# Kernel optimization log

Hardware: AMD Instinct MI355X
Metric: run time of the kernel (lower is better)

The kernel has to match this reference:

```python
import jax, jax.numpy as jnp
import numpy as np

EMB = 1024
HEADS = 16
HEAD_DIM = EMB // HEADS


def setup_inputs() -> dict:
    key = jax.random.key(0)
    ks = jax.random.split(key, 6)
    B, T, D = 4, 2048, EMB
    s = 1.0 / np.sqrt(D)
    return {
        "x": jax.random.normal(ks[0], (B, T, D), dtype=jnp.float32),
        "Wq": jax.random.normal(ks[1], (D, D), dtype=jnp.float32) * s,
        "Wk": jax.random.normal(ks[2], (D, D), dtype=jnp.float32) * s,
        "Wv": jax.random.normal(ks[3], (D, D), dtype=jnp.float32) * s,
        "Wo": jax.random.normal(ks[4], (D, D), dtype=jnp.float32) * s,
        "bo": jax.random.normal(ks[5], (D,), dtype=jnp.float32) * 0.01,
    }


def reference(x, Wq, Wk, Wv, Wo, bo):
    B, T, D = x.shape
    H, Hd = HEADS, HEAD_DIM
    # torch Linear: x @ W.T ; here W stored [out,in]
    def heads(W):
        return (x @ W.T).reshape(B, T, H, Hd).transpose(0, 2, 1, 3)  # [B,H,T,Hd]
    Q, K, V = heads(Wq), heads(Wk), heads(Wv)
    scores = jnp.einsum("bhqd,bhkd->bhqk", Q, K) / np.sqrt(Hd)
    causal = jnp.triu(jnp.ones((T, T), dtype=bool), k=1)
    scores = jnp.where(causal, -jnp.inf, scores)
    weights = jax.nn.softmax(scores, axis=-1)  # dropout rate 0 -> identity
    ctx = jnp.einsum("bhqk,bhkd->bhqd", weights, V)
    ctx = ctx.transpose(0, 2, 1, 3).reshape(B, T, D)
    return ctx @ Wo.T + bo
```

## Files before the change

### kernel.cpp

```cpp
#include <hip/hip_runtime.h>

typedef short bf16x8 __attribute__((ext_vector_type(8)));
typedef float f32x4 __attribute__((ext_vector_type(4)));
typedef unsigned short u16;
typedef unsigned int u32;

__device__ __forceinline__ u16 f2b(float x) {
  union { float f; u32 u; } c; c.f = x;
  u32 r = (c.u + 0x7FFFu + ((c.u >> 16) & 1u)) >> 16;
  return (u16)r;
}

__device__ __forceinline__ float fexp2(float x) {
  return __builtin_amdgcn_exp2f(x);
}

__device__ __forceinline__ void glds16(const void* g, void* l) {
  __builtin_amdgcn_global_load_lds(
      (const __attribute__((address_space(1))) u32*)g,
      (__attribute__((address_space(3))) u32*)l, 16, 0, 0);
}

__global__ void cvt_kernel(const float* __restrict__ src, u16* __restrict__ dst,
                           int n4, float scale) {
  int i = blockIdx.x * blockDim.x + threadIdx.x;
  if (i >= n4) return;
  float4 v = reinterpret_cast<const float4*>(src)[i];
  ushort4 o;
  o.x = f2b(v.x * scale); o.y = f2b(v.y * scale);
  o.z = f2b(v.z * scale); o.w = f2b(v.w * scale);
  reinterpret_cast<ushort4*>(dst)[i] = o;
}

template<int MODE>
__global__ __launch_bounds__(256, 2)
void gemm_bt(const u16* __restrict__ A, const u16* __restrict__ Bm,
             u16* __restrict__ Cq, u16* __restrict__ Ck, u16* __restrict__ Cv,
             float* __restrict__ Cf, const float* __restrict__ bias, int K) {
  __shared__ __attribute__((aligned(16))) u16 As[128 * 32];
  __shared__ __attribute__((aligned(16))) u16 Bs[128 * 32];
  const int tid = threadIdx.x;
  const int w = tid >> 6, l = tid & 63;
  const int wr = w >> 1, wc = w & 1;
  const int lr = l & 15, lg = l >> 4;
  const int row0 = blockIdx.x * 128;
  const int col0 = blockIdx.y * 128;
  const int sr = l >> 2;
  const int sc = (l & 3) * 8;

  f32x4 acc[4][4] = {};

  for (int kt = 0; kt < K; kt += 32) {
    __syncthreads();
#pragma unroll
    for (int cc = 0; cc < 2; ++cc) {
      const int c = w * 2 + cc;
      glds16(A + (size_t)(row0 + c * 16 + sr) * K + kt + sc, &As[c * 512]);
      glds16(Bm + (size_t)(col0 + c * 16 + sr) * K + kt + sc, &Bs[c * 512]);
    }
    asm volatile("s_waitcnt vmcnt(0)" ::: "memory");
    __syncthreads();

    bf16x8 af[4], bfr[4];
#pragma unroll
    for (int m = 0; m < 4; ++m)
      af[m] = *reinterpret_cast<const bf16x8*>(&As[(wr * 64 + m * 16 + lr) * 32 + lg * 8]);
#pragma unroll
    for (int n = 0; n < 4; ++n)
      bfr[n] = *reinterpret_cast<const bf16x8*>(&Bs[(wc * 64 + n * 16 + lr) * 32 + lg * 8]);
#pragma unroll
    for (int m = 0; m < 4; ++m)
#pragma unroll
      for (int n = 0; n < 4; ++n)
        acc[m][n] = __builtin_amdgcn_mfma_f32_16x16x32_bf16(af[m], bfr[n], acc[m][n], 0, 0, 0);
  }

  if (MODE == 0) {
    const int seg = col0 >> 10;
    u16* dst = (seg == 0) ? Cq : (seg == 1 ? Ck : Cv);
    const int cseg = col0 & 1023;
#pragma unroll
    for (int m = 0; m < 4; ++m) {
      const size_t r = (size_t)(row0 + wr * 64 + m * 16 + lg * 4);
#pragma unroll
      for (int n = 0; n < 4; ++n) {
        const int cg = cseg + wc * 64 + n * 16 + lr;
#pragma unroll
        for (int j = 0; j < 4; ++j)
          dst[(r + j) * 1024 + cg] = f2b(acc[m][n][j]);
      }
    }
  } else {
#pragma unroll
    for (int m = 0; m < 4; ++m) {
      const size_t r = (size_t)(row0 + wr * 64 + m * 16 + lg * 4);
#pragma unroll
      for (int n = 0; n < 4; ++n) {
        const int cg = col0 + wc * 64 + n * 16 + lr;
        const float bv = bias[cg];
#pragma unroll
        for (int j = 0; j < 4; ++j)
          Cf[(r + j) * 1024 + cg] = acc[m][n][j] + bv;
      }
    }
  }
}

__global__ void transpose_v(const u16* __restrict__ vb, u16* __restrict__ vt) {
  __shared__ __attribute__((aligned(16))) u16 Ls[64][72];
  const int bh = blockIdx.x, tb = blockIdx.y;
  const int bb = bh >> 4, h = bh & 15;
  const int t0 = tb * 64;
  const int tid = threadIdx.x;
#pragma unroll
  for (int it = 0; it < 2; ++it) {
    int idx = it * 256 + tid;
    int r = idx >> 3, c8 = (idx & 7) * 8;
    *reinterpret_cast<bf16x8*>(&Ls[r][c8]) =
        *reinterpret_cast<const bf16x8*>(&vb[(size_t)(bb * 2048 + t0 + r) * 1024 + h * 64 + c8]);
  }
  __syncthreads();
#pragma unroll
  for (int it = 0; it < 2; ++it) {
    int idx = it * 256 + tid;
    int d = idx >> 3, c8 = (idx & 7) * 8;
    bf16x8 v;
#pragma unroll
    for (int i = 0; i < 8; ++i) v[i] = (short)Ls[c8 + i][d];
    *reinterpret_cast<bf16x8*>(&vt[(size_t)(bh * 64 + d) * 2048 + t0 + c8]) = v;
  }
}

__global__ __launch_bounds__(256, 3)
void attn_kernel(const u16* __restrict__ qb, const u16* __restrict__ kb,
                 const u16* __restrict__ vt, u16* __restrict__ ctx) {
  __shared__ __attribute__((aligned(16))) u16 Ks[2][64 * 72];
  __shared__ __attribute__((aligned(16))) u16 Vs[2][64 * 72];
  __shared__ __attribute__((aligned(16))) u16 Ps[4 * 32 * 64];
  const int bid = blockIdx.x;
  const int qt = 15 - (bid >> 6);
  const int bh = bid & 63;
  const int bb = bh >> 4, h = bh & 15;
  const int tid = threadIdx.x, w = tid >> 6, l = tid & 63;
  const int lr = l & 15, lg = l >> 4;
  const int Qw = qt * 128 + w * 32;
  const int kvr = tid >> 3;
  const int kvc = (tid & 7) * 8;

  bf16x8 qf[2][2];
#pragma unroll
  for (int mi = 0; mi < 2; ++mi)
#pragma unroll
    for (int kc = 0; kc < 2; ++kc)
      qf[mi][kc] = *reinterpret_cast<const bf16x8*>(
          &qb[(size_t)(bb * 2048 + Qw + mi * 16 + lr) * 1024 + h * 64 + kc * 32 + lg * 8]);

  f32x4 oacc[2][4] = {};
  float lsum[2][4] = {};

  const int ntiles = 2 * qt + 2;

  bf16x8 kr[2], vr[2];
#pragma unroll
  for (int it = 0; it < 2; ++it) {
    kr[it] = *reinterpret_cast<const bf16x8*>(
        &kb[(size_t)(bb * 2048 + it * 32 + kvr) * 1024 + h * 64 + kvc]);
    vr[it] = *reinterpret_cast<const bf16x8*>(
        &vt[(size_t)(bh * 64 + it * 32 + kvr) * 2048 + kvc]);
  }
#pragma unroll
  for (int it = 0; it < 2; ++it) {
    *reinterpret_cast<bf16x8*>(&Ks[0][(it * 32 + kvr) * 72 + kvc]) = kr[it];
    *reinterpret_cast<bf16x8*>(&Vs[0][(it * 32 + kvr) * 72 + kvc]) = vr[it];
  }
  __syncthreads();
#pragma unroll
  for (int it = 0; it < 2; ++it) {
    kr[it] = *reinterpret_cast<const bf16x8*>(
        &kb[(size_t)(bb * 2048 + 64 + it * 32 + kvr) * 1024 + h * 64 + kvc]);
    vr[it] = *reinterpret_cast<const bf16x8*>(
        &vt[(size_t)(bh * 64 + it * 32 + kvr) * 2048 + 64 + kvc]);
  }

  for (int t = 0; t < ntiles; ++t) {
    const int c0 = t * 64;
    const int cur = t & 1;

    if (c0 < Qw + 32) {
      const bool diag = (c0 + 63 > Qw);

      f32x4 sacc[2][4] = {};
      __builtin_amdgcn_s_setprio(1);
#pragma unroll
      for (int kc = 0; kc < 2; ++kc)
#pragma unroll
        for (int nj = 0; nj < 4; ++nj) {
          bf16x8 kf = *reinterpret_cast<const bf16x8*>(
              &Ks[cur][(nj * 16 + lr) * 72 + kc * 32 + lg * 8]);
#pragma unroll
          for (int mi = 0; mi < 2; ++mi)
            sacc[mi][nj] = __builtin_amdgcn_mfma_f32_16x16x32_bf16(qf[mi][kc], kf, sacc[mi][nj], 0, 0, 0);
        }
      __builtin_amdgcn_s_setprio(0);

#pragma unroll
      for (int mi = 0; mi < 2; ++mi) {
        if (diag) {
#pragma unroll
          for (int nj = 0; nj < 4; ++nj) {
            const int col = c0 + nj * 16 + lr;
#pragma unroll
            for (int j = 0; j < 4; ++j) {
              const int row = Qw + mi * 16 + lg * 4 + j;
              if (col > row) sacc[mi][nj][j] = -1e30f;
            }
          }
        }
#pragma unroll
        for (int nj = 0; nj < 4; ++nj) {
          const int cchunk = nj * 2 + (lr >> 3);
          const int coff = lr & 7;
#pragma unroll
          for (int j = 0; j < 4; ++j) {
            const float p = fexp2(sacc[mi][nj][j]);
            lsum[mi][j] += p;
            const int rowP = mi * 16 + lg * 4 + j;
            Ps[w * 2048 + rowP * 64 + ((cchunk ^ (rowP & 7)) * 8) + coff] = f2b(p);
          }
        }
      }

      __builtin_amdgcn_s_setprio(1);
#pragma unroll
      for (int kc = 0; kc < 2; ++kc) {
        bf16x8 pf[2];
#pragma unroll
        for (int mi = 0; mi < 2; ++mi) {
          const int rowP = mi * 16 + lr;
          const int cj = kc * 4 + lg;
          pf[mi] = *reinterpret_cast<const bf16x8*>(
              &Ps[w * 2048 + rowP * 64 + ((cj ^ (rowP & 7)) * 8)]);
        }
#pragma unroll
        for (int nd = 0; nd < 4; ++nd) {
          bf16x8 vf = *reinterpret_cast<const bf16x8*>(
              &Vs[cur][(nd * 16 + lr) * 72 + kc * 32 + lg * 8]);
#pragma unroll
          for (int mi = 0; mi < 2; ++mi)
            oacc[mi][nd] = __builtin_amdgcn_mfma_f32_16x16x32_bf16(pf[mi], vf, oacc[mi][nd], 0, 0, 0);
        }
      }
      __builtin_amdgcn_s_setprio(0);
    }

    if (t + 1 < ntiles) {
#pragma unroll
      for (int it = 0; it < 2; ++it) {
        *reinterpret_cast<bf16x8*>(&Ks[cur ^ 1][(it * 32 + kvr) * 72 + kvc]) = kr[it];
        *reinterpret_cast<bf16x8*>(&Vs[cur ^ 1][(it * 32 + kvr) * 72 + kvc]) = vr[it];
      }
    }
    __syncthreads();
    if (t + 2 < ntiles) {
      const int c0n = c0 + 128;
#pragma unroll
      for (int it = 0; it < 2; ++it) {
        kr[it] = *reinterpret_cast<const bf16x8*>(
            &kb[(size_t)(bb * 2048 + c0n + it * 32 + kvr) * 1024 + h * 64 + kvc]);
        vr[it] = *reinterpret_cast<const bf16x8*>(
            &vt[(size_t)(bh * 64 + it * 32 + kvr) * 2048 + c0n + kvc]);
      }
    }
  }

#pragma unroll
  for (int mi = 0; mi < 2; ++mi) {
#pragma unroll
    for (int x = 1; x < 16; x <<= 1)
#pragma unroll
      for (int j = 0; j < 4; ++j) lsum[mi][j] += __shfl_xor(lsum[mi][j], x, 64);
#pragma unroll
    for (int j = 0; j < 4; ++j) {
      const float inv = 1.0f / lsum[mi][j];
      const size_t r = (size_t)(bb * 2048 + Qw + mi * 16 + lg * 4 + j);
#pragma unroll
      for (int nd = 0; nd < 4; ++nd)
        ctx[r * 1024 + h * 64 + nd * 16 + lr] = f2b(oacc[mi][nd][j] * inv);
    }
  }
}

extern "C" void kernel_launch(void* const* d_in, const int* in_sizes, int n_in,
                              void* d_out, int out_size, void* d_ws, size_t ws_size,
                              hipStream_t stream) {
  const float* x = (const float*)d_in[0];
  const float* Wq = (const float*)d_in[1];
  const float* Wk = (const float*)d_in[2];
  const float* Wv = (const float*)d_in[3];
  const float* Wo = (const float*)d_in[4];
  const float* bo = (const float*)d_in[5];
  float* out = (float*)d_out;

  char* ws = (char*)d_ws;
  u16* xb = (u16*)(ws);
  u16* qb = (u16*)(ws + (16u << 20));
  u16* kb = (u16*)(ws + (32u << 20));
  u16* vb = (u16*)(ws + (48u << 20));
  u16* vtb = (u16*)(ws + (64u << 20));
  u16* wqkvb = (u16*)(ws + (80u << 20));
  u16* wob = (u16*)(ws + (88u << 20));

  const float qscale = 0.125f * 1.4426950408889634f;
  cvt_kernel<<<8192, 256, 0, stream>>>(x, xb, 8388608 / 4, 1.0f);
  cvt_kernel<<<1024, 256, 0, stream>>>(Wq, wqkvb, 1048576 / 4, qscale);
  cvt_kernel<<<1024, 256, 0, stream>>>(Wk, wqkvb + 1048576, 1048576 / 4, 1.0f);
  cvt_kernel<<<1024, 256, 0, stream>>>(Wv, wqkvb + 2097152, 1048576 / 4, 1.0f);
  cvt_kernel<<<1024, 256, 0, stream>>>(Wo, wob, 1048576 / 4, 1.0f);

  gemm_bt<0><<<dim3(64, 24), 256, 0, stream>>>(xb, wqkvb, qb, kb, vb, nullptr, nullptr, 1024);
  transpose_v<<<dim3(64, 32), 256, 0, stream>>>(vb, vtb);
  attn_kernel<<<1024, 256, 0, stream>>>(qb, kb, vtb, xb);
  gemm_bt<1><<<dim3(64, 8), 256, 0, stream>>>(xb, wob, nullptr, nullptr, nullptr, out, bo, 1024);
}
```

Baseline: 176.3 us.

## Rewrite GEMMs with triple-buffered swizzled LDS pipeline and fuse V transpose

Replaces the simple single-buffered 128x128 GEMM with a 512-thread, 128x256-tile kernel. It stages 64-wide K slices through a three-deep LDS ring using async global-to-LDS loads, XOR-swizzled layout, split MFMA phases and priority hints, so global loads overlap compute and LDS bank conflicts drop. The QKV GEMM epilogue now writes V directly in transposed per-head layout, which removes the separate transpose kernel and its round trip through memory. The cost is that the transposed V stores are scattered 2-byte writes, and the larger tiles mean fewer blocks in the grid.

```diff
diff --git a/kernel.cpp b/kernel.cpp
--- a/kernel.cpp
+++ b/kernel.cpp
@@ -33,101 +33,183 @@
 }
 
 template<int MODE>
-__global__ __launch_bounds__(256, 2)
-void gemm_bt(const u16* __restrict__ A, const u16* __restrict__ Bm,
-             u16* __restrict__ Cq, u16* __restrict__ Ck, u16* __restrict__ Cv,
-             float* __restrict__ Cf, const float* __restrict__ bias, int K) {
-  __shared__ __attribute__((aligned(16))) u16 As[128 * 32];
-  __shared__ __attribute__((aligned(16))) u16 Bs[128 * 32];
+__global__ __launch_bounds__(512, 2)
+void gemm2(const u16* __restrict__ A, const u16* __restrict__ Bm,
+           u16* __restrict__ Cq, u16* __restrict__ Ck, u16* __restrict__ Cvt,
+           float* __restrict__ Cf, const float* __restrict__ bias) {
+  constexpr int K = 1024, NKT = K / 64;
+  __shared__ __attribute__((aligned(16))) u16 lds[3][24576];
   const int tid = threadIdx.x;
-  const int w = tid >> 6, l = tid & 63;
-  const int wr = w >> 1, wc = w & 1;
+  const int w = tid >> 6;
+  const int l = tid & 63;
+  const int wm = w >> 2, wn = w & 3;
   const int lr = l & 15, lg = l >> 4;
-  const int row0 = blockIdx.x * 128;
-  const int col0 = blockIdx.y * 128;
-  const int sr = l >> 2;
-  const int sc = (l & 3) * 8;
+  const int brow = blockIdx.x * 128;
+  const int bcol = blockIdx.y * 256;
+  const int wg = w * 64;
+
+  const u16* Ab = A + (size_t)brow * K;
+  const u16* Bb = Bm + (size_t)bcol * K;
+  int gA[2], lA[2], gB[4], lB[4];
+#pragma unroll
+  for (int i = 0; i < 2; ++i) {
+    const int q = i * 512 + tid;
+    const int r = q >> 3, s = (q & 7) ^ (r & 7);
+    gA[i] = r * K + s * 8;
+    lA[i] = (i * 512 + wg) * 8;
+  }
+#pragma unroll
+  for (int i = 0; i < 4; ++i) {
+    const int q = i * 512 + tid;
+    const int r = q >> 3, s = (q & 7) ^ (r & 7);
+    gB[i] = r * K + s * 8;
+    lB[i] = 8192 + (i * 512 + wg) * 8;
+  }
+
+  int aoff[4][2], boff[4][2];
+#pragma unroll
+  for (int m = 0; m < 4; ++m) {
+    const int row = wm * 64 + m * 16 + lr;
+#pragma unroll
+    for (int kk = 0; kk < 2; ++kk)
+      aoff[m][kk] = row * 64 + (((kk * 4 + lg) ^ (row & 7)) * 8);
+  }
+#pragma unroll
+  for (int n = 0; n < 4; ++n) {
+    const int row = wn * 64 + n * 16 + lr;
+#pragma unroll
+    for (int kk = 0; kk < 2; ++kk)
+      boff[n][kk] = 8192 + row * 64 + (((kk * 4 + lg) ^ (row & 7)) * 8);
+  }
 
   f32x4 acc[4][4] = {};
 
-  for (int kt = 0; kt < K; kt += 32) {
-    __syncthreads();
-#pragma unroll
-    for (int cc = 0; cc < 2; ++cc) {
-      const int c = w * 2 + cc;
-      glds16(A + (size_t)(row0 + c * 16 + sr) * K + kt + sc, &As[c * 512]);
-      glds16(Bm + (size_t)(col0 + c * 16 + sr) * K + kt + sc, &Bs[c * 512]);
-    }
-    asm volatile("s_waitcnt vmcnt(0)" ::: "memory");
-    __syncthreads();
-
-    bf16x8 af[4], bfr[4];
+#pragma unroll
+  for (int i = 0; i < 2; ++i) glds16(Ab + gA[i], &lds[0][lA[i]]);
+#pragma unroll
+  for (int i = 0; i < 4; ++i) glds16(Bb + gB[i], &lds[0][lB[i]]);
+#pragma unroll
+  for (int i = 0; i < 2; ++i) glds16(Ab + gA[i] + 64, &lds[1][lA[i]]);
+#pragma unroll
+  for (int i = 0; i < 4; ++i) glds16(Bb + gB[i] + 64, &lds[1][lB[i]]);
+  asm volatile("s_waitcnt vmcnt(6)" ::: "memory");
+  asm volatile("s_barrier" ::: "memory");
+
+  int bi = 0;
+  for (int kt = 0; kt < NKT; ++kt) {
+    const u16* Lb = lds[bi];
+    const int bs = (bi + 2 >= 3) ? (bi - 1) : (bi + 2);
+    const bool st = (kt + 2 < NKT);
+    const int ko = (kt + 2) * 64;
+
+    bf16x8 a[4][2], b01[2][2];
 #pragma unroll
     for (int m = 0; m < 4; ++m)
-      af[m] = *reinterpret_cast<const bf16x8*>(&As[(wr * 64 + m * 16 + lr) * 32 + lg * 8]);
-#pragma unroll
-    for (int n = 0; n < 4; ++n)
-      bfr[n] = *reinterpret_cast<const bf16x8*>(&Bs[(wc * 64 + n * 16 + lr) * 32 + lg * 8]);
+#pragma unroll
+      for (int kk = 0; kk < 2; ++kk)
+        a[m][kk] = *reinterpret_cast<const bf16x8*>(&Lb[aoff[m][kk]]);
+#pragma unroll
+    for (int n = 0; n < 2; ++n)
+#pragma unroll
+      for (int kk = 0; kk < 2; ++kk)
+        b01[n][kk] = *reinterpret_cast<const bf16x8*>(&Lb[boff[n][kk]]);
+    if (st) {
+      glds16(Ab + gA[0] + ko, &lds[bs][lA[0]]);
+      glds16(Ab + gA[1] + ko, &lds[bs][lA[1]]);
+      glds16(Bb + gB[0] + ko, &lds[bs][lB[0]]);
+    }
+    asm volatile("s_barrier" ::: "memory");
+    asm volatile("s_waitcnt lgkmcnt(0)" ::: "memory");
+    __builtin_amdgcn_sched_barrier(0);
+    __builtin_amdgcn_s_setprio(1);
 #pragma unroll
     for (int m = 0; m < 4; ++m)
 #pragma unroll
-      for (int n = 0; n < 4; ++n)
-        acc[m][n] = __builtin_amdgcn_mfma_f32_16x16x32_bf16(af[m], bfr[n], acc[m][n], 0, 0, 0);
+      for (int n = 0; n < 2; ++n)
+#pragma unroll
+        for (int kk = 0; kk < 2; ++kk)
+          acc[m][n] = __builtin_amdgcn_mfma_f32_16x16x32_bf16(a[m][kk], b01[n][kk], acc[m][n], 0, 0, 0);
+    __builtin_amdgcn_s_setprio(0);
+    asm volatile("s_barrier" ::: "memory");
+
+    bf16x8 b23[2][2];
+#pragma unroll
+    for (int n = 0; n < 2; ++n)
+#pragma unroll
+      for (int kk = 0; kk < 2; ++kk)
+        b23[n][kk] = *reinterpret_cast<const bf16x8*>(&Lb[boff[n + 2][kk]]);
+    if (st) {
+      glds16(Bb + gB[1] + ko, &lds[bs][lB[1]]);
+      glds16(Bb + gB[2] + ko, &lds[bs][lB[2]]);
+      glds16(Bb + gB[3] + ko, &lds[bs][lB[3]]);
+    }
+    if (kt + 1 < NKT) {
+      if (st) asm volatile("s_waitcnt vmcnt(6)" ::: "memory");
+      else    asm volatile("s_waitcnt vmcnt(0)" ::: "memory");
+    }
+    asm volatile("s_barrier" ::: "memory");
+    asm volatile("s_waitcnt lgkmcnt(0)" ::: "memory");
+    __builtin_amdgcn_sched_barrier(0);
+    __builtin_amdgcn_s_setprio(1);
+#pragma unroll
+    for (int m = 0; m < 4; ++m)
+#pragma unroll
+      for (int n = 0; n < 2; ++n)
+#pragma unroll
+        for (int kk = 0; kk < 2; ++kk)
+          acc[m][n + 2] = __builtin_amdgcn_mfma_f32_16x16x32_bf16(a[m][kk], b23[n][kk], acc[m][n + 2], 0, 0, 0);
+    __builtin_amdgcn_s_setprio(0);
+    asm volatile("s_barrier" ::: "memory");
+
+    bi = (bi + 1 >= 3) ? 0 : bi + 1;
   }
 
   if (MODE == 0) {
-    const int seg = col0 >> 10;
-    u16* dst = (seg == 0) ? Cq : (seg == 1 ? Ck : Cv);
-    const int cseg = col0 & 1023;
+    const int seg = blockIdx.y >> 2;
+    const int cbase = (blockIdx.y & 3) * 256;
+    if (seg < 2) {
+      u16* dst = (seg == 0) ? Cq : Ck;
+#pragma unroll
+      for (int m = 0; m < 4; ++m) {
+        const size_t r = (size_t)(brow + wm * 64 + m * 16 + lg * 4);
+#pragma unroll
+        for (int n = 0; n < 4; ++n) {
+          const int c = cbase + wn * 64 + n * 16 + lr;
+#pragma unroll
+          for (int j = 0; j < 4; ++j)
+            dst[(r + j) * 1024 + c] = f2b(acc[m][n][j]);
+        }
+      }
+    } else {
+#pragma unroll
+      for (int n = 0; n < 4; ++n) {
+        const int c = cbase + wn * 64 + n * 16 + lr;
+        const int hh = c >> 6, dd = c & 63;
+#pragma unroll
+        for (int m = 0; m < 4; ++m) {
+          const int r0 = brow + wm * 64 + m * 16 + lg * 4;
+#pragma unroll
+          for (int j = 0; j < 4; ++j) {
+            const int r = r0 + j;
+            const int bt = r >> 11, tt = r & 2047;
+            Cvt[((size_t)((bt * 16 + hh) * 64 + dd)) * 2048 + tt] = f2b(acc[m][n][j]);
+          }
+        }
+      }
+    }
+  } else {
 #pragma unroll
     for (int m = 0; m < 4; ++m) {
-      const size_t r = (size_t)(row0 + wr * 64 + m * 16 + lg * 4);
+      const size_t r = (size_t)(brow + wm * 64 + m * 16 + lg * 4);
 #pragma unroll
       for (int n = 0; n < 4; ++n) {
-        const int cg = cseg + wc * 64 + n * 16 + lr;
+        const int c = bcol + wn * 64 + n * 16 + lr;
+        const float bv = bias[c];
 #pragma unroll
         for (int j = 0; j < 4; ++j)
-          dst[(r + j) * 1024 + cg] = f2b(acc[m][n][j]);
-      }
-    }
-  } else {
-#pragma unroll
-    for (int m = 0; m < 4; ++m) {
-      const size_t r = (size_t)(row0 + wr * 64 + m * 16 + lg * 4);
-#pragma unroll
-      for (int n = 0; n < 4; ++n) {
-        const int cg = col0 + wc * 64 + n * 16 + lr;
-        const float bv = bias[cg];
-#pragma unroll
-        for (int j = 0; j < 4; ++j)
-          Cf[(r + j) * 1024 + cg] = acc[m][n][j] + bv;
-      }
-    }
-  }
-}
-
-__global__ void transpose_v(const u16* __restrict__ vb, u16* __restrict__ vt) {
-  __shared__ __attribute__((aligned(16))) u16 Ls[64][72];
-  const int bh = blockIdx.x, tb = blockIdx.y;
-  const int bb = bh >> 4, h = bh & 15;
-  const int t0 = tb * 64;
-  const int tid = threadIdx.x;
-#pragma unroll
-  for (int it = 0; it < 2; ++it) {
-    int idx = it * 256 + tid;
-    int r = idx >> 3, c8 = (idx & 7) * 8;
-    *reinterpret_cast<bf16x8*>(&Ls[r][c8]) =
-        *reinterpret_cast<const bf16x8*>(&vb[(size_t)(bb * 2048 + t0 + r) * 1024 + h * 64 + c8]);
-  }
-  __syncthreads();
-#pragma unroll
-  for (int it = 0; it < 2; ++it) {
-    int idx = it * 256 + tid;
-    int d = idx >> 3, c8 = (idx & 7) * 8;
-    bf16x8 v;
-#pragma unroll
-    for (int i = 0; i < 8; ++i) v[i] = (short)Ls[c8 + i][d];
-    *reinterpret_cast<bf16x8*>(&vt[(size_t)(bh * 64 + d) * 2048 + t0 + c8]) = v;
+          Cf[(r + j) * 1024 + c] = acc[m][n][j] + bv;
+      }
+    }
   }
 }
 
@@ -305,7 +387,6 @@
   u16* xb = (u16*)(ws);
   u16* qb = (u16*)(ws + (16u << 20));
   u16* kb = (u16*)(ws + (32u << 20));
-  u16* vb = (u16*)(ws + (48u << 20));
   u16* vtb = (u16*)(ws + (64u << 20));
   u16* wqkvb = (u16*)(ws + (80u << 20));
   u16* wob = (u16*)(ws + (88u << 20));
@@ -317,8 +398,7 @@
   cvt_kernel<<<1024, 256, 0, stream>>>(Wv, wqkvb + 2097152, 1048576 / 4, 1.0f);
   cvt_kernel<<<1024, 256, 0, stream>>>(Wo, wob, 1048576 / 4, 1.0f);
 
-  gemm_bt<0><<<dim3(64, 24), 256, 0, stream>>>(xb, wqkvb, qb, kb, vb, nullptr, nullptr, 1024);
-  transpose_v<<<dim3(64, 32), 256, 0, stream>>>(vb, vtb);
+  gemm2<0><<<dim3(64, 12), 512, 0, stream>>>(xb, wqkvb, qb, kb, vtb, nullptr, nullptr);
   attn_kernel<<<1024, 256, 0, stream>>>(qb, kb, vtb, xb);
-  gemm_bt<1><<<dim3(64, 8), 256, 0, stream>>>(xb, wob, nullptr, nullptr, nullptr, out, bo, 1024);
-}
+  gemm2<1><<<dim3(64, 4), 512, 0, stream>>>(xb, wob, nullptr, nullptr, nullptr, out, bo);
+}
```

Result: faster. 166.4 us (-5.6%).
